# Performance work log

Hardware: AMD Instinct MI355X
Metric: run time of the kernel (lower is better)

The kernel has to match this reference:

```python
import jax, jax.numpy as jnp
import numpy as np

N, S, H, B = 4096, 128, 768, 128  # hypotheses, seq_len, hidden, utterances
NBEST = N // B


def _seg_softmax(x, seg, num_segments):
    # softmax within each n-best group (segments along last axis of a 1-D vector)
    m = jax.ops.segment_max(x, seg, num_segments=num_segments)
    ex = jnp.exp(x - m[seg])
    s = jax.ops.segment_sum(ex, seg, num_segments=num_segments)
    return ex / s[seg]


def setup_inputs() -> dict:
    key = jax.random.key(0)
    ks = jax.random.split(key, 6)
    pooler_output = jax.random.normal(ks[0], (N, H), jnp.float32)
    last_hidden_state = jax.random.normal(ks[1], (N, S, H), jnp.float32)
    attention_mask = jnp.ones((N, S), jnp.float32)
    am_score = jax.random.normal(ks[2], (N, 1), jnp.float32)
    ctc_score = jax.random.normal(ks[3], (N, 1), jnp.float32)
    # one-hot label: first hypothesis of each n-best group is the oracle
    labels = jnp.zeros((N,), jnp.float32).at[jnp.arange(B) * NBEST].set(1.0)
    W = jax.random.normal(ks[4], (H + 2, 1), jnp.float32) * 0.02
    b = jnp.zeros((1,), jnp.float32)
    nBestIndex = jnp.full((B,), NBEST, jnp.int32)  # group sizes
    return {
        'pooler_output': pooler_output,
        'last_hidden_state': last_hidden_state,
        'attention_mask': attention_mask,
        'am_score': am_score,
        'ctc_score': ctc_score,
        'labels': labels,
        'W': W,
        'b': b,
        'nBestIndex': nBestIndex,
    }


def reference(pooler_output, last_hidden_state, attention_mask, am_score,
              ctc_score, labels, W, b, nBestIndex):
    num_seg = nBestIndex.shape[0]
    n = pooler_output.shape[0]
    seg = jnp.repeat(jnp.arange(num_seg), nBestIndex, total_repeat_length=n)

    # AvgPooling: masked mean over sequence -> [N, H]
    pooled = (last_hidden_state * attention_mask[..., None]).sum(axis=1) \
             / attention_mask.sum(axis=1, keepdims=True)

    # concat pooler with am/ctc scores -> [N, 770], linear -> scalar score per hyp
    concat_state = jnp.concatenate([pooler_output, am_score, ctc_score], axis=-1)
    final_score = (concat_state @ W + b).squeeze(-1)  # [N]

    # segmented (n-best) softmax over scores, then CE loss against one-hot labels
    final_prob = _seg_softmax(final_score, seg, num_seg)
    ce_loss = -jnp.sum(labels * jnp.log(final_prob)) / n

    # similarity matrix between pooler outputs and avg-pooled embeddings [N, N]
    sim = jnp.einsum('id,jd->ij', pooler_output, pooled)
    # per-row segmented softmax (vectorized version of the original Python loop)
    sim_prob = jax.vmap(lambda r: _seg_softmax(r, seg, num_seg))(sim)
    contrast_loss = -jnp.sum(jnp.diagonal(sim_prob)) / num_seg

    loss = ce_loss + contrast_loss
    return final_score, loss
```

## Files before the change

kernel.cpp:

```cpp
#include <hip/hip_runtime.h>
#include <math.h>

typedef float f32x4 __attribute__((ext_vector_type(4)));


__global__ void seg_kernel(const int* __restrict__ nbest,
                           int* __restrict__ starts, int* __restrict__ seg,
                           float* __restrict__ loss, int B) {
    __shared__ int sh[1025];
    const int t = threadIdx.x;
    for (int g = t; g < B; g += blockDim.x) sh[g] = nbest[g];
    __syncthreads();
    if (t == 0) {
        int off = 0;
        for (int g = 0; g < B; ++g) { int v = sh[g]; sh[g] = off; off += v; }
        sh[B] = off;
        *loss = 0.f;
    }
    __syncthreads();
    for (int g = t; g <= B; g += blockDim.x) starts[g] = sh[g];
    for (int g = t; g < B; g += blockDim.x) {
        const int s0 = sh[g], s1 = sh[g + 1];
        for (int i = s0; i < s1; ++i) seg[i] = g;
    }
}

__global__ __launch_bounds__(256, 4)
void pool_kernel_h768(const float* __restrict__ lhs,
                      const float* __restrict__ mask,
                      const float* __restrict__ pooler,
                      const float* __restrict__ am,
                      const float* __restrict__ ctc,
                      const float* __restrict__ W,
                      const float* __restrict__ bb,
                      float* __restrict__ pooled,
                      float* __restrict__ score,
                      int N, int S) {
    const int H  = 768;
    const int Hv = 192;
    const int wid  = threadIdx.x >> 6;
    const int lane = threadIdx.x & 63;
    const int j = blockIdx.x * 4 + wid;
    if (j >= N) return;

    const f32x4* row  = (const f32x4*)(lhs + (size_t)j * S * H) + lane;
    const float* mrow = mask + (size_t)j * S;

    f32x4 a0 = {0.f,0.f,0.f,0.f}, a1 = a0, a2 = a0;
    float msum = 0.f;
#pragma unroll 8
    for (int s = 0; s < S; ++s) {
        float m = mrow[s];
        const f32x4* p = row + (size_t)s * Hv;
        f32x4 v0 = __builtin_nontemporal_load(p);
        f32x4 v1 = __builtin_nontemporal_load(p + 64);
        f32x4 v2 = __builtin_nontemporal_load(p + 128);
        a0 += v0 * m; a1 += v1 * m; a2 += v2 * m;
        msum += m;
    }
    const float inv = 1.0f / msum;
    f32x4* prow = (f32x4*)(pooled + (size_t)j * H);
    prow[lane]       = a0 * inv;
    prow[lane + 64]  = a1 * inv;
    prow[lane + 128] = a2 * inv;

    const f32x4* pr = (const f32x4*)(pooler + (size_t)j * H);
    const f32x4* Wv = (const f32x4*)W;
    float acc = 0.f;
#pragma unroll
    for (int k = lane; k < Hv; k += 64) {
        f32x4 p = pr[k] * Wv[k];
        acc += p.x + p.y + p.z + p.w;
    }
    for (int d = 32; d > 0; d >>= 1) acc += __shfl_xor(acc, d, 64);
    if (lane == 0)
        score[j] = acc + am[j] * W[H] + ctc[j] * W[H + 1] + bb[0];
}

__global__ void pool_kernel_generic(const float* __restrict__ lhs,
                                    const float* __restrict__ mask,
                                    const float* __restrict__ pooler,
                                    const float* __restrict__ am,
                                    const float* __restrict__ ctc,
                                    const float* __restrict__ W,
                                    const float* __restrict__ bb,
                                    float* __restrict__ pooled,
                                    float* __restrict__ score,
                                    int S, int H) {
    const int j  = blockIdx.x;
    const int t  = threadIdx.x;
    const int Hv = H >> 2;
    const f32x4* row  = (const f32x4*)(lhs + (size_t)j * S * H);
    const float* mrow = mask + (size_t)j * S;
    f32x4 acc = {0.f,0.f,0.f,0.f};
    float msum = 0.f;
#pragma unroll 4
    for (int s = 0; s < S; ++s) {
        float m = mrow[s];
        acc += __builtin_nontemporal_load(&row[(size_t)s * Hv + t]) * m;
        msum += m;
    }
    ((f32x4*)(pooled + (size_t)j * H))[t] = acc * (1.0f / msum);
    if (t < 64) {
        const f32x4* pr = (const f32x4*)(pooler + (size_t)j * H);
        const f32x4* Wv = (const f32x4*)W;
        float a = 0.f;
        for (int k = t; k < Hv; k += 64) {
            f32x4 p = pr[k] * Wv[k];
            a += p.x + p.y + p.z + p.w;
        }
        for (int d = 32; d > 0; d >>= 1) a += __shfl_xor(a, d, 64);
        if (t == 0)
            score[j] = a + am[j] * W[H] + ctc[j] * W[H + 1] + bb[0];
    }
}

__global__ void finale_kernel(const float* __restrict__ pooler,
                              const float* __restrict__ pooled,
                              const float* __restrict__ score,
                              const float* __restrict__ labels,
                              const int* __restrict__ starts,
                              const int* __restrict__ seg,
                              float* __restrict__ loss,
                              int H, int N, int B) {
    const int bid = blockIdx.x;
    if (bid >= N) {
        const int g = bid - N;
        const int lane = threadIdx.x;
        if (lane >= 64) return;
        const int s0 = starts[g], sz = starts[g + 1] - s0;
        float m = -INFINITY;
        for (int idx = lane; idx < sz; idx += 64) m = fmaxf(m, score[s0 + idx]);
        for (int d = 32; d > 0; d >>= 1) m = fmaxf(m, __shfl_xor(m, d, 64));
        float s = 0.f;
        for (int idx = lane; idx < sz; idx += 64) s += expf(score[s0 + idx] - m);
        for (int d = 32; d > 0; d >>= 1) s += __shfl_xor(s, d, 64);
        const float ls = logf(s);
        float c = 0.f;
        for (int idx = lane; idx < sz; idx += 64) {
            float lb = labels[s0 + idx];
            if (lb != 0.f) c += lb * (score[s0 + idx] - m - ls);
        }
        for (int d = 32; d > 0; d >>= 1) c += __shfl_xor(c, d, 64);
        if (lane == 0) atomicAdd(loss, -c / (float)N);
        return;
    }
    __shared__ float simv[512];
    const int i  = bid;
    const int g  = seg[i];
    const int s0 = starts[g], sz = starts[g + 1] - s0;
    const int wid = threadIdx.x >> 6, lane = threadIdx.x & 63;
    const int nw  = blockDim.x >> 6;
    const int Hv  = H >> 2;
    const f32x4* pi = (const f32x4*)(pooler + (size_t)i * H);
    for (int j = wid; j < sz; j += nw) {
        const f32x4* pj = (const f32x4*)(pooled + (size_t)(s0 + j) * H);
        float acc = 0.f;
        for (int k = lane; k < Hv; k += 64) {
            f32x4 p = pi[k] * pj[k];
            acc += p.x + p.y + p.z + p.w;
        }
        for (int d = 32; d > 0; d >>= 1) acc += __shfl_xor(acc, d, 64);
        if (lane == 0) simv[j] = acc;
    }
    __syncthreads();
    if (wid == 0) {
        float m = -INFINITY;
        for (int idx = lane; idx < sz; idx += 64) m = fmaxf(m, simv[idx]);
        for (int d = 32; d > 0; d >>= 1) m = fmaxf(m, __shfl_xor(m, d, 64));
        float s = 0.f;
        for (int idx = lane; idx < sz; idx += 64) s += expf(simv[idx] - m);
        for (int d = 32; d > 0; d >>= 1) s += __shfl_xor(s, d, 64);
        if (lane == 0) {
            const int p = i - s0;
            const float prob = expf(simv[p] - m) / s;
            atomicAdd(loss, -prob / (float)B);
        }
    }
}

extern "C" void kernel_launch(void* const* d_in, const int* in_sizes, int n_in,
                              void* d_out, int out_size, void* d_ws, size_t ws_size,
                              hipStream_t stream) {
    const float* pooler = (const float*)d_in[0];
    const float* lhs    = (const float*)d_in[1];
    const float* mask   = (const float*)d_in[2];
    const float* am     = (const float*)d_in[3];
    const float* ctc    = (const float*)d_in[4];
    const float* labels = (const float*)d_in[5];
    const float* W      = (const float*)d_in[6];
    const float* bb     = (const float*)d_in[7];
    const int*   nbest  = (const int*)d_in[8];

    const int N = in_sizes[5];
    const int B = in_sizes[8];
    const int H = in_sizes[0] / N;
    const int S = in_sizes[2] / N;

    float* out  = (float*)d_out;
    float* loss = out + N;

    float* pooled = (float*)d_ws;
    int*   starts = (int*)((char*)d_ws + (size_t)N * H * sizeof(float));
    int*   seg    = starts + (B + 1);

    hipLaunchKernelGGL(seg_kernel, dim3(1), dim3(256), 0, stream,
                       nbest, starts, seg, loss, B);
    if (H == 768) {
        hipLaunchKernelGGL(pool_kernel_h768, dim3((N + 3) / 4), dim3(256), 0,
                           stream, lhs, mask, pooler, am, ctc, W, bb,
                           pooled, out, N, S);
    } else {
        hipLaunchKernelGGL(pool_kernel_generic, dim3(N), dim3(H / 4), 0,
                           stream, lhs, mask, pooler, am, ctc, W, bb,
                           pooled, out, S, H);
    }
    hipLaunchKernelGGL(finale_kernel, dim3(N + B), dim3(256), 0, stream,
                       pooler, pooled, out, labels, starts, seg, loss, H, N, B);
}
```

Baseline: 327.6 us.

## Replace per-row finale with per-group kernel staging pooled rows in LDS

```diff
diff --git a/kernel.cpp b/kernel.cpp
--- a/kernel.cpp
+++ b/kernel.cpp
@@ -3,27 +3,6 @@
 
 typedef float f32x4 __attribute__((ext_vector_type(4)));
 
-
-__global__ void seg_kernel(const int* __restrict__ nbest,
-                           int* __restrict__ starts, int* __restrict__ seg,
-                           float* __restrict__ loss, int B) {
-    __shared__ int sh[1025];
-    const int t = threadIdx.x;
-    for (int g = t; g < B; g += blockDim.x) sh[g] = nbest[g];
-    __syncthreads();
-    if (t == 0) {
-        int off = 0;
-        for (int g = 0; g < B; ++g) { int v = sh[g]; sh[g] = off; off += v; }
-        sh[B] = off;
-        *loss = 0.f;
-    }
-    __syncthreads();
-    for (int g = t; g <= B; g += blockDim.x) starts[g] = sh[g];
-    for (int g = t; g < B; g += blockDim.x) {
-        const int s0 = sh[g], s1 = sh[g + 1];
-        for (int i = s0; i < s1; ++i) seg[i] = g;
-    }
-}
 
 __global__ __launch_bounds__(256, 4)
 void pool_kernel_h768(const float* __restrict__ lhs,
@@ -38,6 +17,8 @@
                       int N, int S) {
     const int H  = 768;
     const int Hv = 192;
+    if (blockIdx.x == 0 && threadIdx.x == 0) score[N] = 0.f;
+
     const int wid  = threadIdx.x >> 6;
     const int lane = threadIdx.x & 63;
     const int j = blockIdx.x * 4 + wid;
@@ -75,6 +56,170 @@
     for (int d = 32; d > 0; d >>= 1) acc += __shfl_xor(acc, d, 64);
     if (lane == 0)
         score[j] = acc + am[j] * W[H] + ctc[j] * W[H + 1] + bb[0];
+}
+
+#define MAX_ROWS 40
+#define PADV 193
+
+__global__ __launch_bounds__(256)
+void group_kernel(const float* __restrict__ pooler,
+                  const float* __restrict__ pooled,
+                  const float* __restrict__ score,
+                  const float* __restrict__ labels,
+                  const int* __restrict__ nbest,
+                  float* __restrict__ loss,
+                  int N, int B) {
+    __shared__ f32x4 s_pool[MAX_ROWS * PADV];
+    __shared__ int   s_nb[1024];
+    __shared__ int   sh_s0, sh_sz;
+    __shared__ float blk_loss;
+
+    const int g = blockIdx.x;
+    const int t = threadIdx.x;
+
+    for (int i = t; i < B; i += 256) s_nb[i] = nbest[i];
+    __syncthreads();
+    if (t == 0) {
+        int off = 0;
+        for (int i = 0; i < g; ++i) off += s_nb[i];
+        sh_s0 = off; sh_sz = s_nb[g];
+        blk_loss = 0.f;
+    }
+    __syncthreads();
+    const int s0 = sh_s0, sz = sh_sz;
+
+    const f32x4* pooled4 = (const f32x4*)pooled;
+    const bool staged = (sz <= MAX_ROWS);
+    if (staged) {
+        for (int idx = t; idx < sz * 192; idx += 256) {
+            int r = idx / 192, c = idx - r * 192;
+            s_pool[r * PADV + c] = pooled4[(size_t)(s0 + r) * 192 + c];
+        }
+    }
+    __syncthreads();
+
+    const int wid  = t >> 6;
+    const int lane = t & 63;
+    const f32x4* jbase  = staged ? s_pool : (pooled4 + (size_t)s0 * 192);
+    const int    jstride = staged ? PADV : 192;
+
+    if (sz <= 32) {
+        const int jj = lane & 31, half = lane >> 5;
+        for (int p = 0; wid + 8 * p < sz; ++p) {
+            const int  r   = wid + 8 * p + 4 * half;
+            const bool rok = (r < sz);
+            const bool jok = (jj < sz);
+            const f32x4* pi = (const f32x4*)(pooler + (size_t)(s0 + (rok ? r : 0)) * 768);
+            const f32x4* pj = jbase + (size_t)(jok ? jj : 0) * jstride;
+            f32x4 accA = {0.f,0.f,0.f,0.f}, accB = accA;
+#pragma unroll 4
+            for (int k = 0; k < 192; k += 2) {
+                accA += pi[k]     * pj[k];
+                accB += pi[k + 1] * pj[k + 1];
+            }
+            f32x4 acc4 = accA + accB;
+            float val = (rok && jok) ? (acc4.x + acc4.y + acc4.z + acc4.w)
+                                     : -INFINITY;
+            float m = val;
+            for (int d = 1; d < 32; d <<= 1) m = fmaxf(m, __shfl_xor(m, d, 64));
+            float e = (rok && jok) ? expf(val - m) : 0.f;
+            float ssum = e;
+            for (int d = 1; d < 32; d <<= 1) ssum += __shfl_xor(ssum, d, 64);
+            if (rok && jok && jj == r)
+                atomicAdd(&blk_loss, -(e / ssum) / (float)B);
+        }
+    } else if (sz <= 64) {
+        for (int r = wid; r < sz; r += 4) {
+            const bool jok = (lane < sz);
+            const f32x4* pi = (const f32x4*)(pooler + (size_t)(s0 + r) * 768);
+            const f32x4* pj = jbase + (size_t)(jok ? lane : 0) * jstride;
+            f32x4 accA = {0.f,0.f,0.f,0.f}, accB = accA;
+#pragma unroll 4
+            for (int k = 0; k < 192; k += 2) {
+                accA += pi[k]     * pj[k];
+                accB += pi[k + 1] * pj[k + 1];
+            }
+            f32x4 acc4 = accA + accB;
+            float val = jok ? (acc4.x + acc4.y + acc4.z + acc4.w) : -INFINITY;
+            float m = val;
+            for (int d = 1; d < 64; d <<= 1) m = fmaxf(m, __shfl_xor(m, d, 64));
+            float e = jok ? expf(val - m) : 0.f;
+            float ssum = e;
+            for (int d = 1; d < 64; d <<= 1) ssum += __shfl_xor(ssum, d, 64);
+            if (jok && lane == r)
+                atomicAdd(&blk_loss, -(e / ssum) / (float)B);
+        }
+    } else {
+        for (int r = wid; r < sz; r += 4) {
+            const f32x4* pi = (const f32x4*)(pooler + (size_t)(s0 + r) * 768);
+            float mrun = -INFINITY, srun = 0.f, dval = 0.f;
+            for (int jc = 0; jc < sz; jc += 64) {
+                const int  j   = jc + lane;
+                const bool jok = (j < sz);
+                const f32x4* pj = pooled4 + (size_t)(s0 + (jok ? j : 0)) * 192;
+                f32x4 accA = {0.f,0.f,0.f,0.f}, accB = accA;
+                for (int k = 0; k < 192; k += 2) {
+                    accA += pi[k]     * pj[k];
+                    accB += pi[k + 1] * pj[k + 1];
+                }
+                f32x4 acc4 = accA + accB;
+                float val = jok ? (acc4.x + acc4.y + acc4.z + acc4.w) : -INFINITY;
+                float cm = val;
+                for (int d = 1; d < 64; d <<= 1) cm = fmaxf(cm, __shfl_xor(cm, d, 64));
+                float e = jok ? expf(val - cm) : 0.f;
+                float cs = e;
+                for (int d = 1; d < 64; d <<= 1) cs += __shfl_xor(cs, d, 64);
+                float nm = fmaxf(mrun, cm);
+                srun = srun * expf(mrun - nm) + cs * expf(cm - nm);
+                float dv = __shfl(val, r - jc, 64);
+                if (r >= jc && r < jc + 64) dval = dv;
+                mrun = nm;
+            }
+            if (lane == 0)
+                atomicAdd(&blk_loss, -(expf(dval - mrun) / srun) / (float)B);
+        }
+    }
+
+    __syncthreads();
+    if (wid == 0) {
+        float m = -INFINITY;
+        for (int idx = lane; idx < sz; idx += 64) m = fmaxf(m, score[s0 + idx]);
+        for (int d = 1; d < 64; d <<= 1) m = fmaxf(m, __shfl_xor(m, d, 64));
+        float s = 0.f;
+        for (int idx = lane; idx < sz; idx += 64) s += expf(score[s0 + idx] - m);
+        for (int d = 1; d < 64; d <<= 1) s += __shfl_xor(s, d, 64);
+        const float ls = logf(s);
+        float c = 0.f;
+        for (int idx = lane; idx < sz; idx += 64) {
+            float lb = labels[s0 + idx];
+            if (lb != 0.f) c += lb * (score[s0 + idx] - m - ls);
+        }
+        for (int d = 1; d < 64; d <<= 1) c += __shfl_xor(c, d, 64);
+        if (lane == 0) atomicAdd(&blk_loss, -c / (float)N);
+    }
+    __syncthreads();
+    if (t == 0) atomicAdd(loss, blk_loss);
+}
+
+__global__ void seg_kernel(const int* __restrict__ nbest,
+                           int* __restrict__ starts, int* __restrict__ seg,
+                           float* __restrict__ loss, int B) {
+    __shared__ int sh[1025];
+    const int t = threadIdx.x;
+    for (int g = t; g < B; g += blockDim.x) sh[g] = nbest[g];
+    __syncthreads();
+    if (t == 0) {
+        int off = 0;
+        for (int g = 0; g < B; ++g) { int v = sh[g]; sh[g] = off; off += v; }
+        sh[B] = off;
+        *loss = 0.f;
+    }
+    __syncthreads();
+    for (int g = t; g <= B; g += blockDim.x) starts[g] = sh[g];
+    for (int g = t; g < B; g += blockDim.x) {
+        const int s0 = sh[g], s1 = sh[g + 1];
+        for (int i = s0; i < s1; ++i) seg[i] = g;
+    }
 }
 
 __global__ void pool_kernel_generic(const float* __restrict__ lhs,
@@ -199,22 +344,24 @@
 
     float* out  = (float*)d_out;
     float* loss = out + N;
-
     float* pooled = (float*)d_ws;
-    int*   starts = (int*)((char*)d_ws + (size_t)N * H * sizeof(float));
-    int*   seg    = starts + (B + 1);
-
-    hipLaunchKernelGGL(seg_kernel, dim3(1), dim3(256), 0, stream,
-                       nbest, starts, seg, loss, B);
+
     if (H == 768) {
         hipLaunchKernelGGL(pool_kernel_h768, dim3((N + 3) / 4), dim3(256), 0,
                            stream, lhs, mask, pooler, am, ctc, W, bb,
                            pooled, out, N, S);
+        hipLaunchKernelGGL(group_kernel, dim3(B), dim3(256), 0, stream,
+                           pooler, pooled, out, labels, nbest, loss, N, B);
     } else {
+        int* starts = (int*)((char*)d_ws + (size_t)N * H * sizeof(float));
+        int* seg    = starts + (B + 1);
+        hipLaunchKernelGGL(seg_kernel, dim3(1), dim3(256), 0, stream,
+                           nbest, starts, seg, loss, B);
         hipLaunchKernelGGL(pool_kernel_generic, dim3(N), dim3(H / 4), 0,
                            stream, lhs, mask, pooler, am, ctc, W, bb,
                            pooled, out, S, H);
-    }
-    hipLaunchKernelGGL(finale_kernel, dim3(N + B), dim3(256), 0, stream,
-                       pooler, pooled, out, labels, starts, seg, loss, H, N, B);
-}
+        hipLaunchKernelGGL(finale_kernel, dim3(N + B), dim3(256), 0, stream,
+                           pooler, pooled, out, labels, starts, seg, loss,
+                           H, N, B);
+    }
+}
```

After: 304.6 us. 7.0% less time.
